# Kernel optimization log

Hardware: AMD Instinct MI355X
Metric: run time of the kernel (lower is better)

Reference implementation:

```python
import jax, jax.numpy as jnp
import numpy as np

TAU = 2.0          # LIF membrane time constant (spikingjelly default)
V_TH = 1.0         # v_threshold
V_RESET = 0.0      # hard reset value
ATAN_ALPHA = 2.0   # surrogate.ATan default alpha
EPS = 1e-12        # F.normalize eps

@jax.custom_vjp
def spike_fn(x):
    # Heaviside forward, ATan surrogate backward
    return (x >= 0).astype(x.dtype)

def _spike_fwd(x):
    return spike_fn(x), x

def _spike_bwd(x, g):
    sg = (ATAN_ALPHA / 2.0) / (1.0 + (jnp.pi / 2.0 * ATAN_ALPHA * x) ** 2)
    return (g * sg,)

spike_fn.defvjp(_spike_fwd, _spike_bwd)

def setup_inputs() -> dict:
    key = jax.random.key(0)
    k1, k2 = jax.random.split(key)
    T, B, F, H = 32, 512, 2048, 2048
    x_seq = jax.random.normal(k1, (T, B, F), dtype=jnp.float32)
    lim = float(np.sqrt(6.0 / (F + H)))  # xavier_uniform
    W = jax.random.uniform(k2, (H, F), dtype=jnp.float32, minval=-lim, maxval=lim)
    b = jnp.zeros((H,), dtype=jnp.float32)
    return {"x_seq": x_seq, "W": W, "b": b}

def reference(x_seq, W, b):
    # Linear: [T,B,F] @ [F,H] -> [T,B,H]
    cur = jnp.einsum('tbf,hf->tbh', x_seq, W) + b
    # F.normalize(dim=-1): L2 normalize the injected current per neuron vector
    norm = jnp.maximum(jnp.sqrt(jnp.sum(cur * cur, axis=-1, keepdims=True)), EPS)
    cur = cur / norm

    def step(v, c):
        # LIF charge: v <- v + (x - (v - v_reset)) / tau
        v = v + (c - (v - V_RESET)) / TAU
        s = spike_fn(v - V_TH)
        sd = jax.lax.stop_gradient(s)  # detach_reset=True
        v = v * (1.0 - sd) + V_RESET * sd  # hard reset
        return v, s

    v0 = jnp.zeros(cur.shape[1:], dtype=cur.dtype)  # [B,H]
    _, spk_seq = jax.lax.scan(step, v0, cur)  # spk_seq: [T,B,H]
    count = spk_seq.sum(axis=0)  # [B,H]
    return spk_seq, count
```

## Files before the change

kernel.cpp:

```cpp
#include <hip/hip_runtime.h>
#include <hip/hip_bf16.h>

#define T_SZ 32
#define B_SZ 512
#define F_SZ 2048
#define H_SZ 2048
#define M_SZ (T_SZ * B_SZ)

#define BM 256
#define BN 256
#define BK 128
#define NT (F_SZ / BK)
#define BUF_BYTES  65536
#define HALF_BYTES 16384

typedef int   i32x8  __attribute__((ext_vector_type(8)));
typedef float f32x16 __attribute__((ext_vector_type(16)));

__device__ __forceinline__ void gload_lds16(const void* g, void* l) {
    __builtin_amdgcn_global_load_lds(
        (const __attribute__((address_space(1))) unsigned int*)g,
        (__attribute__((address_space(3))) unsigned int*)l,
        16, 0, 0);
}

__device__ __forceinline__ float bf16_bits_to_f32(unsigned short u) {
    return __uint_as_float(((unsigned)u) << 16);
}

__device__ __forceinline__ void sbar() {
    __builtin_amdgcn_sched_barrier(0);
    __builtin_amdgcn_s_barrier();
    __builtin_amdgcn_sched_barrier(0);
}

__device__ __forceinline__ void stage_half_tile(unsigned char* lds,
                                                const unsigned char* gpanel,
                                                int kbyte, int tid) {
    #pragma unroll
    for (int j = 0; j < 2; ++j) {
        int c   = j * 512 + tid;
        int row = c >> 3;
        int u   = (c & 7) ^ (row & 7);
        gload_lds16(gpanel + (size_t)row * F_SZ + kbyte + u * 16, (void*)(lds + c * 16));
    }
}

__global__ __launch_bounds__(256) void cvt_fp8_kernel(const float* __restrict__ in,
                                                      unsigned int* __restrict__ out,
                                                      float scale, int n8) {
    int i = blockIdx.x * 256 + threadIdx.x;
    if (i >= n8) return;
    float4 v0 = ((const float4*)in)[2 * i];
    float4 v1 = ((const float4*)in)[2 * i + 1];
    int w0 = __builtin_amdgcn_cvt_pk_fp8_f32(v0.x * scale, v0.y * scale, 0, false);
    w0     = __builtin_amdgcn_cvt_pk_fp8_f32(v0.z * scale, v0.w * scale, w0, true);
    int w1 = __builtin_amdgcn_cvt_pk_fp8_f32(v1.x * scale, v1.y * scale, 0, false);
    w1     = __builtin_amdgcn_cvt_pk_fp8_f32(v1.z * scale, v1.w * scale, w1, true);
    ((uint2*)out)[i] = make_uint2((unsigned)w0, (unsigned)w1);
}

__global__ __launch_bounds__(256) void init_ss_kernel(float4* __restrict__ ss4) {
    ss4[blockIdx.x * 256 + threadIdx.x] = make_float4(0.f, 0.f, 0.f, 0.f);
}

__global__ __launch_bounds__(512, 2) void gemm_fp8_kernel(const unsigned char* __restrict__ A,
                                                          const unsigned char* __restrict__ Bt,
                                                          const float* __restrict__ bias,
                                                          __hip_bfloat16* __restrict__ C,
                                                          float* __restrict__ ss)
{
    __shared__ __align__(16) unsigned char smem[2 * BUF_BYTES];

    const int tid  = threadIdx.x;
    const int lane = tid & 63;
    const int wave = tid >> 6;
    const int wm   = wave >> 2;
    const int wn   = wave & 3;
    const int l31  = lane & 31;
    const int kh   = lane >> 5;

    const int flat = blockIdx.y * 8 + blockIdx.x;
    const int swz  = (flat & 7) * 64 + (flat >> 3);
    const int n0   = (swz & 7) * BN;
    const int m0   = (swz >> 3) * BM;

    f32x16 acc[4][2] = {};

    stage_half_tile(smem + 32768,              Bt + (size_t)(n0      ) * F_SZ, 0, tid);
    stage_half_tile(smem + 32768 + HALF_BYTES, Bt + (size_t)(n0 + 128) * F_SZ, 0, tid);
    stage_half_tile(smem,                      A  + (size_t)(m0      ) * F_SZ, 0, tid);
    stage_half_tile(smem + HALF_BYTES,         A  + (size_t)(m0 + 128) * F_SZ, 0, tid);
    stage_half_tile(smem + BUF_BYTES + 32768,              Bt + (size_t)(n0      ) * F_SZ, BK, tid);
    stage_half_tile(smem + BUF_BYTES + 32768 + HALF_BYTES, Bt + (size_t)(n0 + 128) * F_SZ, BK, tid);
    asm volatile("s_waitcnt vmcnt(4)" ::: "memory");
    sbar();

    #pragma unroll 1
    for (int kt = 0; kt < NT; ++kt) {
        const int cur = kt & 1;
        const int nxt = cur ^ 1;
        unsigned char* const As = smem + cur * BUF_BYTES;
        unsigned char* const Bs = As + 32768;

        auto read_af = [&](i32x8* dst, int mi) {
            const int ra = wm * 128 + mi * 32 + l31;
            #pragma unroll
            for (int s = 0; s < 2; ++s) {
                const int ua = s * 4 + kh * 2;
                ((int4*)&dst[s])[0] = *(const int4*)(As + ra * BK + (((ua + 0) ^ (ra & 7)) * 16));
                ((int4*)&dst[s])[1] = *(const int4*)(As + ra * BK + (((ua + 1) ^ (ra & 7)) * 16));
            }
        };

        i32x8 bq[2][2];
        #pragma unroll
        for (int ni = 0; ni < 2; ++ni) {
            const int rb = wn * 64 + ni * 32 + l31;
            #pragma unroll
            for (int s = 0; s < 2; ++s) {
                const int ua = s * 4 + kh * 2;
                ((int4*)&bq[ni][s])[0] = *(const int4*)(Bs + rb * BK + (((ua + 0) ^ (rb & 7)) * 16));
                ((int4*)&bq[ni][s])[1] = *(const int4*)(Bs + rb * BK + (((ua + 1) ^ (rb & 7)) * 16));
            }
        }
        i32x8 af[2][2];
        read_af(af[0], 0);

        #pragma unroll
        for (int mi = 0; mi < 4; ++mi) {
            if (mi < 3) read_af(af[(mi + 1) & 1], mi + 1);

            if (mi == 0 && kt < NT - 1)
                stage_half_tile(smem + nxt * BUF_BYTES,              A  + (size_t)(m0      ) * F_SZ, (kt + 1) * BK, tid);
            if (mi == 1 && kt < NT - 1)
                stage_half_tile(smem + nxt * BUF_BYTES + HALF_BYTES, A  + (size_t)(m0 + 128) * F_SZ, (kt + 1) * BK, tid);
            if (mi == 2 && kt < NT - 2)
                stage_half_tile(smem + cur * BUF_BYTES + 32768,              Bt + (size_t)(n0      ) * F_SZ, (kt + 2) * BK, tid);
            if (mi == 3 && kt < NT - 2)
                stage_half_tile(smem + cur * BUF_BYTES + 32768 + HALF_BYTES, Bt + (size_t)(n0 + 128) * F_SZ, (kt + 2) * BK, tid);

            __builtin_amdgcn_sched_barrier(0);
            __builtin_amdgcn_s_setprio(1);
            #pragma unroll
            for (int ni = 0; ni < 2; ++ni)
                #pragma unroll
                for (int s = 0; s < 2; ++s)
                    acc[mi][ni] = __builtin_amdgcn_mfma_scale_f32_32x32x64_f8f6f4(
                        af[mi & 1][s], bq[ni][s], acc[mi][ni],
                        0 , 0 ,
                        0, 0x7f7f7f7f,
                        0, 0x7f7f7f7f);
            __builtin_amdgcn_s_setprio(0);
            if (mi < 3) sbar();
        }

        if (kt <= NT - 3)      { asm volatile("s_waitcnt vmcnt(4)" ::: "memory"); }
        else if (kt == NT - 2) { asm volatile("s_waitcnt vmcnt(0)" ::: "memory"); }
        sbar();
    }

    float bv[2];
    #pragma unroll
    for (int ni = 0; ni < 2; ++ni) bv[ni] = bias[n0 + wn * 64 + ni * 32 + l31];
    #pragma unroll
    for (int mi = 0; mi < 4; ++mi) {
        const int gmb = m0 + wm * 128 + mi * 32 + 4 * kh;
        #pragma unroll
        for (int r = 0; r < 16; ++r) {
            const int grow = gmb + (r & 3) + 8 * (r >> 2);
            float p = 0.f;
            #pragma unroll
            for (int ni = 0; ni < 2; ++ni) {
                const int gn = n0 + wn * 64 + ni * 32 + l31;
                const float val = acc[mi][ni][r] * (1.0f / 256.0f) + bv[ni];
                C[(size_t)grow * H_SZ + gn] = __float2bfloat16(val);
                p += val * val;
            }
            p += __shfl_xor(p, 1, 64);
            p += __shfl_xor(p, 2, 64);
            p += __shfl_xor(p, 4, 64);
            p += __shfl_xor(p, 8, 64);
            p += __shfl_xor(p, 16, 64);
            if (l31 == 0) atomicAdd(ss + grow, p);
        }
    }
}

__global__ __launch_bounds__(256) void lif_scan_kernel(const __hip_bfloat16* __restrict__ cur,
                                                       const float* __restrict__ ss,
                                                       float* __restrict__ spk,
                                                       float* __restrict__ cnt)
{
    __shared__ float s_inv[T_SZ];
    const int gid = blockIdx.x * 256 + threadIdx.x;
    const int b   = gid >> 9;
    const int h0  = (gid & 511) * 4;

    if (threadIdx.x < T_SZ)
        s_inv[threadIdx.x] = 1.0f / fmaxf(sqrtf(ss[threadIdx.x * B_SZ + b]), 1e-12f);
    __syncthreads();

    const size_t stride = (size_t)B_SZ * H_SZ;
    const size_t base   = (size_t)b * H_SZ + h0;
    const __hip_bfloat16* p = cur + base;

    ushort4 pk[3];
    pk[0] = *(const ushort4*)(p);
    pk[1] = *(const ushort4*)(p + stride);
    pk[2] = *(const ushort4*)(p + 2 * stride);

    float v[4]  = {0, 0, 0, 0};
    float cn[4] = {0, 0, 0, 0};
    #pragma unroll
    for (int t = 0; t < T_SZ; ++t) {
        const ushort4 k = pk[t % 3];
        if (t + 3 < T_SZ) pk[t % 3] = *(const ushort4*)(p + (size_t)(t + 3) * stride);
        const float inv = s_inv[t];
        float so[4];
        {
            float c;
            c = bf16_bits_to_f32(k.x) * inv; v[0] += (c - v[0]) * 0.5f;
            c = bf16_bits_to_f32(k.y) * inv; v[1] += (c - v[1]) * 0.5f;
            c = bf16_bits_to_f32(k.z) * inv; v[2] += (c - v[2]) * 0.5f;
            c = bf16_bits_to_f32(k.w) * inv; v[3] += (c - v[3]) * 0.5f;
        }
        #pragma unroll
        for (int j = 0; j < 4; ++j) {
            float s = (v[j] >= 1.0f) ? 1.0f : 0.0f;
            so[j] = s;
            cn[j] += s;
            v[j] = (s != 0.f) ? 0.f : v[j];
        }
        *(float4*)(spk + base + (size_t)t * stride) = make_float4(so[0], so[1], so[2], so[3]);
    }
    *(float4*)(cnt + base) = make_float4(cn[0], cn[1], cn[2], cn[3]);
}

extern "C" void kernel_launch(void* const* d_in, const int* in_sizes, int n_in,
                              void* d_out, int out_size, void* d_ws, size_t ws_size,
                              hipStream_t stream) {
    const float* x    = (const float*)d_in[0];
    const float* W    = (const float*)d_in[1];
    const float* bias = (const float*)d_in[2];

    float* spk = (float*)d_out;
    float* cnt = spk + (size_t)T_SZ * B_SZ * H_SZ;

    char* ws = (char*)d_ws;
    unsigned char* x8    = (unsigned char*)ws;
    unsigned char* W8    = x8 + (size_t)M_SZ * F_SZ;
    __hip_bfloat16* curb = (__hip_bfloat16*)(W8 + (size_t)H_SZ * F_SZ);
    float* ss            = (float*)((char*)curb + (size_t)M_SZ * H_SZ * 2);

    init_ss_kernel<<<M_SZ / 1024, 256, 0, stream>>>((float4*)ss);
    cvt_fp8_kernel<<<(M_SZ * F_SZ / 8) / 256, 256, 0, stream>>>(x, (unsigned int*)x8, 1.0f,   M_SZ * F_SZ / 8);
    cvt_fp8_kernel<<<(H_SZ * F_SZ / 8) / 256, 256, 0, stream>>>(W, (unsigned int*)W8, 256.0f, H_SZ * F_SZ / 8);
    gemm_fp8_kernel<<<dim3(H_SZ / BN, M_SZ / BM), 512, 0, stream>>>(x8, W8, bias, curb, ss);
    lif_scan_kernel<<<(B_SZ * H_SZ / 4) / 256, 256, 0, stream>>>(curb, ss, spk, cnt);
}
```

Baseline: 372.2 us.

## Shrink FP8 GEMM tile to 256x128x64 with 4 waves and precomputed LDS offsets

Rebuilds the FP8 GEMM mainloop around a smaller 256x128 output tile with BK=64, 256 threads (4 waves, 2x2), and a 4-way XOR swizzle instead of 8-way. Staging and LDS read offsets are computed once before the loop. The per-K schedule is split into two MFMA halves, with the next A tile and the B tile two steps ahead issued between them. The smaller block and LDS footprint aim for more resident blocks and finer-grained latency hiding, at the cost of less operand reuse per block, twice as many K iterations and barriers, and more global traffic for A.

```diff
diff --git a/kernel.cpp b/kernel.cpp
--- a/kernel.cpp
+++ b/kernel.cpp
@@ -8,11 +8,12 @@
 #define M_SZ (T_SZ * B_SZ)
 
 #define BM 256
-#define BN 256
-#define BK 128
+#define BN 128
+#define BK 64
 #define NT (F_SZ / BK)
-#define BUF_BYTES  65536
-#define HALF_BYTES 16384
+#define ABYTES (BM * BK)
+#define BBYTES (BN * BK)
+#define TILE_BYTES (ABYTES + BBYTES)
 
 typedef int   i32x8  __attribute__((ext_vector_type(8)));
 typedef float f32x16 __attribute__((ext_vector_type(16)));
@@ -34,17 +35,8 @@
     __builtin_amdgcn_sched_barrier(0);
 }
 
-__device__ __forceinline__ void stage_half_tile(unsigned char* lds,
-                                                const unsigned char* gpanel,
-                                                int kbyte, int tid) {
-    #pragma unroll
-    for (int j = 0; j < 2; ++j) {
-        int c   = j * 512 + tid;
-        int row = c >> 3;
-        int u   = (c & 7) ^ (row & 7);
-        gload_lds16(gpanel + (size_t)row * F_SZ + kbyte + u * 16, (void*)(lds + c * 16));
-    }
-}
+#define MFMA_FP8(a, b, c) __builtin_amdgcn_mfma_scale_f32_32x32x64_f8f6f4( \
+        (a), (b), (c), 0 , 0 , 0, 0x7f7f7f7f, 0, 0x7f7f7f7f)
 
 __global__ __launch_bounds__(256) void cvt_fp8_kernel(const float* __restrict__ in,
                                                       unsigned int* __restrict__ out,
@@ -64,100 +56,128 @@
     ss4[blockIdx.x * 256 + threadIdx.x] = make_float4(0.f, 0.f, 0.f, 0.f);
 }
 
-__global__ __launch_bounds__(512, 2) void gemm_fp8_kernel(const unsigned char* __restrict__ A,
+__global__ __launch_bounds__(256, 2) void gemm_fp8_kernel(const unsigned char* __restrict__ A,
                                                           const unsigned char* __restrict__ Bt,
                                                           const float* __restrict__ bias,
                                                           __hip_bfloat16* __restrict__ C,
                                                           float* __restrict__ ss)
 {
-    __shared__ __align__(16) unsigned char smem[2 * BUF_BYTES];
+    __shared__ __align__(16) unsigned char smem[2 * TILE_BYTES];
 
     const int tid  = threadIdx.x;
     const int lane = tid & 63;
     const int wave = tid >> 6;
-    const int wm   = wave >> 2;
-    const int wn   = wave & 3;
+    const int wm   = wave >> 1;
+    const int wn   = wave & 1;
     const int l31  = lane & 31;
     const int kh   = lane >> 5;
 
-    const int flat = blockIdx.y * 8 + blockIdx.x;
-    const int swz  = (flat & 7) * 64 + (flat >> 3);
-    const int n0   = (swz & 7) * BN;
-    const int m0   = (swz >> 3) * BM;
+    const int flat = blockIdx.y * 16 + blockIdx.x;
+    const int swz  = (flat & 7) * 128 + (flat >> 3);
+    const int n0   = (swz & 15) * BN;
+    const int m0   = (swz >> 4) * BM;
+
+    const unsigned char* const Ap = A  + (size_t)m0 * F_SZ;
+    const unsigned char* const Bp = Bt + (size_t)n0 * F_SZ;
+
+    int sAg[4], sAl[4];
+    #pragma unroll
+    for (int j = 0; j < 4; ++j) {
+        const int c = j * 256 + tid;
+        const int row = c >> 2;
+        const int u = (c & 3) ^ (row & 3);
+        sAg[j] = row * F_SZ + u * 16;
+        sAl[j] = c * 16;
+    }
+    int sBg[2], sBl[2];
+    #pragma unroll
+    for (int j = 0; j < 2; ++j) {
+        const int c = j * 256 + tid;
+        const int row = c >> 2;
+        const int u = (c & 3) ^ (row & 3);
+        sBg[j] = row * F_SZ + u * 16;
+        sBl[j] = c * 16;
+    }
+
+    int aoff[4][2], boff[2][2];
+    #pragma unroll
+    for (int mi = 0; mi < 4; ++mi) {
+        const int ra = wm * 128 + mi * 32 + l31;
+        #pragma unroll
+        for (int j = 0; j < 2; ++j)
+            aoff[mi][j] = ra * BK + (((kh * 2 + j) ^ (ra & 3)) * 16);
+    }
+    #pragma unroll
+    for (int ni = 0; ni < 2; ++ni) {
+        const int rb = wn * 64 + ni * 32 + l31;
+        #pragma unroll
+        for (int j = 0; j < 2; ++j)
+            boff[ni][j] = rb * BK + (((kh * 2 + j) ^ (rb & 3)) * 16);
+    }
+
+    auto stageA = [&](int p, int kt) {
+        unsigned char* const d = smem + p * TILE_BYTES;
+        #pragma unroll
+        for (int j = 0; j < 4; ++j) gload_lds16(Ap + kt * BK + sAg[j], d + sAl[j]);
+    };
+    auto stageB = [&](int p, int kt) {
+        unsigned char* const d = smem + p * TILE_BYTES + ABYTES;
+        #pragma unroll
+        for (int j = 0; j < 2; ++j) gload_lds16(Bp + kt * BK + sBg[j], d + sBl[j]);
+    };
 
     f32x16 acc[4][2] = {};
 
-    stage_half_tile(smem + 32768,              Bt + (size_t)(n0      ) * F_SZ, 0, tid);
-    stage_half_tile(smem + 32768 + HALF_BYTES, Bt + (size_t)(n0 + 128) * F_SZ, 0, tid);
-    stage_half_tile(smem,                      A  + (size_t)(m0      ) * F_SZ, 0, tid);
-    stage_half_tile(smem + HALF_BYTES,         A  + (size_t)(m0 + 128) * F_SZ, 0, tid);
-    stage_half_tile(smem + BUF_BYTES + 32768,              Bt + (size_t)(n0      ) * F_SZ, BK, tid);
-    stage_half_tile(smem + BUF_BYTES + 32768 + HALF_BYTES, Bt + (size_t)(n0 + 128) * F_SZ, BK, tid);
-    asm volatile("s_waitcnt vmcnt(4)" ::: "memory");
+    stageB(0, 0);
+    stageA(0, 0);
+    stageB(1, 1);
+    asm volatile("s_waitcnt vmcnt(2)" ::: "memory");
     sbar();
 
     #pragma unroll 1
     for (int kt = 0; kt < NT; ++kt) {
-        const int cur = kt & 1;
-        const int nxt = cur ^ 1;
-        unsigned char* const As = smem + cur * BUF_BYTES;
-        unsigned char* const Bs = As + 32768;
-
-        auto read_af = [&](i32x8* dst, int mi) {
-            const int ra = wm * 128 + mi * 32 + l31;
-            #pragma unroll
-            for (int s = 0; s < 2; ++s) {
-                const int ua = s * 4 + kh * 2;
-                ((int4*)&dst[s])[0] = *(const int4*)(As + ra * BK + (((ua + 0) ^ (ra & 7)) * 16));
-                ((int4*)&dst[s])[1] = *(const int4*)(As + ra * BK + (((ua + 1) ^ (ra & 7)) * 16));
-            }
-        };
-
-        i32x8 bq[2][2];
+        unsigned char* const buf = smem + (kt & 1) * TILE_BYTES;
+        unsigned char* const Bs  = buf + ABYTES;
+
+        i32x8 a01[2], a23[2], bq[2];
+
         #pragma unroll
         for (int ni = 0; ni < 2; ++ni) {
-            const int rb = wn * 64 + ni * 32 + l31;
-            #pragma unroll
-            for (int s = 0; s < 2; ++s) {
-                const int ua = s * 4 + kh * 2;
-                ((int4*)&bq[ni][s])[0] = *(const int4*)(Bs + rb * BK + (((ua + 0) ^ (rb & 7)) * 16));
-                ((int4*)&bq[ni][s])[1] = *(const int4*)(Bs + rb * BK + (((ua + 1) ^ (rb & 7)) * 16));
-            }
-        }
-        i32x8 af[2][2];
-        read_af(af[0], 0);
-
-        #pragma unroll
-        for (int mi = 0; mi < 4; ++mi) {
-            if (mi < 3) read_af(af[(mi + 1) & 1], mi + 1);
-
-            if (mi == 0 && kt < NT - 1)
-                stage_half_tile(smem + nxt * BUF_BYTES,              A  + (size_t)(m0      ) * F_SZ, (kt + 1) * BK, tid);
-            if (mi == 1 && kt < NT - 1)
-                stage_half_tile(smem + nxt * BUF_BYTES + HALF_BYTES, A  + (size_t)(m0 + 128) * F_SZ, (kt + 1) * BK, tid);
-            if (mi == 2 && kt < NT - 2)
-                stage_half_tile(smem + cur * BUF_BYTES + 32768,              Bt + (size_t)(n0      ) * F_SZ, (kt + 2) * BK, tid);
-            if (mi == 3 && kt < NT - 2)
-                stage_half_tile(smem + cur * BUF_BYTES + 32768 + HALF_BYTES, Bt + (size_t)(n0 + 128) * F_SZ, (kt + 2) * BK, tid);
-
-            __builtin_amdgcn_sched_barrier(0);
-            __builtin_amdgcn_s_setprio(1);
-            #pragma unroll
-            for (int ni = 0; ni < 2; ++ni)
-                #pragma unroll
-                for (int s = 0; s < 2; ++s)
-                    acc[mi][ni] = __builtin_amdgcn_mfma_scale_f32_32x32x64_f8f6f4(
-                        af[mi & 1][s], bq[ni][s], acc[mi][ni],
-                        0 , 0 ,
-                        0, 0x7f7f7f7f,
-                        0, 0x7f7f7f7f);
-            __builtin_amdgcn_s_setprio(0);
-            if (mi < 3) sbar();
-        }
-
-        if (kt <= NT - 3)      { asm volatile("s_waitcnt vmcnt(4)" ::: "memory"); }
+            ((int4*)&bq[ni])[0] = *(const int4*)(Bs + boff[ni][0]);
+            ((int4*)&bq[ni])[1] = *(const int4*)(Bs + boff[ni][1]);
+        }
+        #pragma unroll
+        for (int mi = 0; mi < 2; ++mi) {
+            ((int4*)&a01[mi])[0] = *(const int4*)(buf + aoff[mi][0]);
+            ((int4*)&a01[mi])[1] = *(const int4*)(buf + aoff[mi][1]);
+        }
+        if (kt + 1 < NT) stageA((kt + 1) & 1, kt + 1);
+
+        __builtin_amdgcn_s_setprio(1);
+        acc[0][0] = MFMA_FP8(a01[0], bq[0], acc[0][0]);
+        acc[0][1] = MFMA_FP8(a01[0], bq[1], acc[0][1]);
+        acc[1][0] = MFMA_FP8(a01[1], bq[0], acc[1][0]);
+        acc[1][1] = MFMA_FP8(a01[1], bq[1], acc[1][1]);
+        __builtin_amdgcn_s_setprio(0);
+        sbar();
+
+        #pragma unroll
+        for (int mi = 0; mi < 2; ++mi) {
+            ((int4*)&a23[mi])[0] = *(const int4*)(buf + aoff[2 + mi][0]);
+            ((int4*)&a23[mi])[1] = *(const int4*)(buf + aoff[2 + mi][1]);
+        }
+        if (kt + 2 < NT) stageB(kt & 1, kt + 2);
+
+        __builtin_amdgcn_s_setprio(1);
+        acc[2][0] = MFMA_FP8(a23[0], bq[0], acc[2][0]);
+        acc[2][1] = MFMA_FP8(a23[0], bq[1], acc[2][1]);
+        acc[3][0] = MFMA_FP8(a23[1], bq[0], acc[3][0]);
+        acc[3][1] = MFMA_FP8(a23[1], bq[1], acc[3][1]);
+        __builtin_amdgcn_s_setprio(0);
+
+        if (kt < NT - 2)       { asm volatile("s_waitcnt vmcnt(2)" ::: "memory"); }
         else if (kt == NT - 2) { asm volatile("s_waitcnt vmcnt(0)" ::: "memory"); }
-        sbar();
+        if (kt < NT - 1) sbar();
     }
 
     float bv[2];
@@ -256,6 +276,6 @@
     init_ss_kernel<<<M_SZ / 1024, 256, 0, stream>>>((float4*)ss);
     cvt_fp8_kernel<<<(M_SZ * F_SZ / 8) / 256, 256, 0, stream>>>(x, (unsigned int*)x8, 1.0f,   M_SZ * F_SZ / 8);
     cvt_fp8_kernel<<<(H_SZ * F_SZ / 8) / 256, 256, 0, stream>>>(W, (unsigned int*)W8, 256.0f, H_SZ * F_SZ / 8);
-    gemm_fp8_kernel<<<dim3(H_SZ / BN, M_SZ / BM), 512, 0, stream>>>(x8, W8, bias, curb, ss);
+    gemm_fp8_kernel<<<dim3(H_SZ / BN, M_SZ / BM), 256, 0, stream>>>(x8, W8, bias, curb, ss);
     lif_scan_kernel<<<(B_SZ * H_SZ / 4) / 256, 256, 0, stream>>>(curb, ss, spk, cnt);
 }
```

Result: no change. 373.3 us (+0.3%).

## Restructure FP8 GEMM main loop into eight k-split phases with per-phase staging

Applied to the files above, without the earlier changes.

Splits each 128-wide K tile into two 64-byte subtiles stored in separate LDS regions with a new 4-chunk XOR swizzle. The inner loop becomes eight phases, each loading one A fragment (and B fragments on the first phase of a subtile), issuing one global-to-LDS copy, and running two MFMAs between barriers. The old scheme that prefetched B two tiles ahead is replaced by a simple double buffer one tile ahead. Offsets are precomputed outside the loop to cut address arithmetic. In exchange there are twice as many barriers per tile plus a full lgkmcnt wait before each MFMA pair, which may serialise LDS reads with compute.

```diff
diff --git a/kernel.cpp b/kernel.cpp
--- a/kernel.cpp
+++ b/kernel.cpp
@@ -11,8 +11,8 @@
 #define BN 256
 #define BK 128
 #define NT (F_SZ / BK)
-#define BUF_BYTES  65536
-#define HALF_BYTES 16384
+#define SUB_BYTES 16384
+#define BUF_BYTES 65536
 
 typedef int   i32x8  __attribute__((ext_vector_type(8)));
 typedef float f32x16 __attribute__((ext_vector_type(16)));
@@ -34,17 +34,12 @@
     __builtin_amdgcn_sched_barrier(0);
 }
 
-__device__ __forceinline__ void stage_half_tile(unsigned char* lds,
-                                                const unsigned char* gpanel,
-                                                int kbyte, int tid) {
-    #pragma unroll
-    for (int j = 0; j < 2; ++j) {
-        int c   = j * 512 + tid;
-        int row = c >> 3;
-        int u   = (c & 7) ^ (row & 7);
-        gload_lds16(gpanel + (size_t)row * F_SZ + kbyte + u * 16, (void*)(lds + c * 16));
-    }
-}
+#define LGKM0 do { asm volatile("s_waitcnt lgkmcnt(0)" ::: "memory"); \
+                   __builtin_amdgcn_sched_barrier(0); } while (0)
+#define VMW(n) asm volatile("s_waitcnt vmcnt(" #n ")" ::: "memory")
+
+#define MFMA_FP8(a, b, c) __builtin_amdgcn_mfma_scale_f32_32x32x64_f8f6f4( \
+        (a), (b), (c), 0 , 0 , 0, 0x7f7f7f7f, 0, 0x7f7f7f7f)
 
 __global__ __launch_bounds__(256) void cvt_fp8_kernel(const float* __restrict__ in,
                                                       unsigned int* __restrict__ out,
@@ -85,79 +80,100 @@
     const int n0   = (swz & 7) * BN;
     const int m0   = (swz >> 3) * BM;
 
+    const unsigned char* const Ap = A  + (size_t)m0 * F_SZ;
+    const unsigned char* const Bp = Bt + (size_t)n0 * F_SZ;
+
+    int gOff[2], lOff[2];
+    #pragma unroll
+    for (int pr = 0; pr < 2; ++pr) {
+        const int idx = pr * 512 + tid;
+        const int row = idx >> 2;
+        const int u   = (idx & 3) ^ ((row >> 1) & 3);
+        gOff[pr] = row * F_SZ + u * 16;
+        lOff[pr] = idx * 16;
+    }
+
+    int aoffb[4][2], boffb[2][2];
+    #pragma unroll
+    for (int mi = 0; mi < 4; ++mi) {
+        const int ra = wm * 128 + mi * 32 + l31;
+        #pragma unroll
+        for (int j = 0; j < 2; ++j)
+            aoffb[mi][j] = ra * 64 + (((kh * 2 + j) ^ ((ra >> 1) & 3)) * 16);
+    }
+    #pragma unroll
+    for (int ni = 0; ni < 2; ++ni) {
+        const int rb = wn * 64 + ni * 32 + l31;
+        #pragma unroll
+        for (int j = 0; j < 2; ++j)
+            boffb[ni][j] = rb * 64 + (((kh * 2 + j) ^ ((rb >> 1) & 3)) * 16);
+    }
+
     f32x16 acc[4][2] = {};
-
-    stage_half_tile(smem + 32768,              Bt + (size_t)(n0      ) * F_SZ, 0, tid);
-    stage_half_tile(smem + 32768 + HALF_BYTES, Bt + (size_t)(n0 + 128) * F_SZ, 0, tid);
-    stage_half_tile(smem,                      A  + (size_t)(m0      ) * F_SZ, 0, tid);
-    stage_half_tile(smem + HALF_BYTES,         A  + (size_t)(m0 + 128) * F_SZ, 0, tid);
-    stage_half_tile(smem + BUF_BYTES + 32768,              Bt + (size_t)(n0      ) * F_SZ, BK, tid);
-    stage_half_tile(smem + BUF_BYTES + 32768 + HALF_BYTES, Bt + (size_t)(n0 + 128) * F_SZ, BK, tid);
-    asm volatile("s_waitcnt vmcnt(4)" ::: "memory");
-    sbar();
+    i32x8 bq[2];
+
+    {
+        unsigned char* const d = smem;
+        #pragma unroll
+        for (int ks = 0; ks < 2; ++ks)
+            #pragma unroll
+            for (int pr = 0; pr < 2; ++pr) {
+                gload_lds16(Ap + ks * 64 + gOff[pr], d + ks * SUB_BYTES + lOff[pr]);
+                gload_lds16(Bp + ks * 64 + gOff[pr], d + 2 * SUB_BYTES + ks * SUB_BYTES + lOff[pr]);
+            }
+        VMW(0);
+        sbar();
+    }
 
     #pragma unroll 1
     for (int kt = 0; kt < NT; ++kt) {
-        const int cur = kt & 1;
-        const int nxt = cur ^ 1;
-        unsigned char* const As = smem + cur * BUF_BYTES;
-        unsigned char* const Bs = As + 32768;
-
-        auto read_af = [&](i32x8* dst, int mi) {
-            const int ra = wm * 128 + mi * 32 + l31;
-            #pragma unroll
-            for (int s = 0; s < 2; ++s) {
-                const int ua = s * 4 + kh * 2;
-                ((int4*)&dst[s])[0] = *(const int4*)(As + ra * BK + (((ua + 0) ^ (ra & 7)) * 16));
-                ((int4*)&dst[s])[1] = *(const int4*)(As + ra * BK + (((ua + 1) ^ (ra & 7)) * 16));
-            }
-        };
-
-        i32x8 bq[2][2];
-        #pragma unroll
-        for (int ni = 0; ni < 2; ++ni) {
-            const int rb = wn * 64 + ni * 32 + l31;
-            #pragma unroll
-            for (int s = 0; s < 2; ++s) {
-                const int ua = s * 4 + kh * 2;
-                ((int4*)&bq[ni][s])[0] = *(const int4*)(Bs + rb * BK + (((ua + 0) ^ (rb & 7)) * 16));
-                ((int4*)&bq[ni][s])[1] = *(const int4*)(Bs + rb * BK + (((ua + 1) ^ (rb & 7)) * 16));
-            }
-        }
-        i32x8 af[2][2];
-        read_af(af[0], 0);
-
-        #pragma unroll
-        for (int mi = 0; mi < 4; ++mi) {
-            if (mi < 3) read_af(af[(mi + 1) & 1], mi + 1);
-
-            if (mi == 0 && kt < NT - 1)
-                stage_half_tile(smem + nxt * BUF_BYTES,              A  + (size_t)(m0      ) * F_SZ, (kt + 1) * BK, tid);
-            if (mi == 1 && kt < NT - 1)
-                stage_half_tile(smem + nxt * BUF_BYTES + HALF_BYTES, A  + (size_t)(m0 + 128) * F_SZ, (kt + 1) * BK, tid);
-            if (mi == 2 && kt < NT - 2)
-                stage_half_tile(smem + cur * BUF_BYTES + 32768,              Bt + (size_t)(n0      ) * F_SZ, (kt + 2) * BK, tid);
-            if (mi == 3 && kt < NT - 2)
-                stage_half_tile(smem + cur * BUF_BYTES + 32768 + HALF_BYTES, Bt + (size_t)(n0 + 128) * F_SZ, (kt + 2) * BK, tid);
-
-            __builtin_amdgcn_sched_barrier(0);
-            __builtin_amdgcn_s_setprio(1);
-            #pragma unroll
-            for (int ni = 0; ni < 2; ++ni)
-                #pragma unroll
-                for (int s = 0; s < 2; ++s)
-                    acc[mi][ni] = __builtin_amdgcn_mfma_scale_f32_32x32x64_f8f6f4(
-                        af[mi & 1][s], bq[ni][s], acc[mi][ni],
-                        0 , 0 ,
-                        0, 0x7f7f7f7f,
-                        0, 0x7f7f7f7f);
-            __builtin_amdgcn_s_setprio(0);
-            if (mi < 3) sbar();
-        }
-
-        if (kt <= NT - 3)      { asm volatile("s_waitcnt vmcnt(4)" ::: "memory"); }
-        else if (kt == NT - 2) { asm volatile("s_waitcnt vmcnt(0)" ::: "memory"); }
-        sbar();
+        const unsigned char* const buf = smem + (kt & 1) * BUF_BYTES;
+        unsigned char* const nb        = smem + ((kt + 1) & 1) * BUF_BYTES;
+        const bool stg = (kt + 1 < NT);
+        const int  kb  = (kt + 1) * BK;
+
+#define STG_A(ks, pr) do { if (stg) gload_lds16(Ap + kb + (ks) * 64 + gOff[pr], \
+                                                nb + (ks) * SUB_BYTES + lOff[pr]); } while (0)
+#define STG_B(ks, pr) do { if (stg) gload_lds16(Bp + kb + (ks) * 64 + gOff[pr], \
+                                                nb + 2 * SUB_BYTES + (ks) * SUB_BYTES + lOff[pr]); } while (0)
+
+#define PHASE(ks, mi, STAGE_STMT, PRE_TRAIL) do {                              \
+        i32x8 aw;                                                              \
+        if ((mi) == 0) {                                                       \
+            const unsigned char* Bb = buf + 2 * SUB_BYTES + (ks) * SUB_BYTES;  \
+            ((int4*)&bq[0])[0] = *(const int4*)(Bb + boffb[0][0]);             \
+            ((int4*)&bq[0])[1] = *(const int4*)(Bb + boffb[0][1]);             \
+            ((int4*)&bq[1])[0] = *(const int4*)(Bb + boffb[1][0]);             \
+            ((int4*)&bq[1])[1] = *(const int4*)(Bb + boffb[1][1]);             \
+        }                                                                      \
+        {                                                                      \
+            const unsigned char* Ab = buf + (ks) * SUB_BYTES;                  \
+            ((int4*)&aw)[0] = *(const int4*)(Ab + aoffb[mi][0]);               \
+            ((int4*)&aw)[1] = *(const int4*)(Ab + aoffb[mi][1]);               \
+        }                                                                      \
+        STAGE_STMT;                                                            \
+        sbar();                        \
+        LGKM0;                                                                 \
+        __builtin_amdgcn_s_setprio(1);                                         \
+        acc[mi][0] = MFMA_FP8(aw, bq[0], acc[mi][0]);                          \
+        acc[mi][1] = MFMA_FP8(aw, bq[1], acc[mi][1]);                          \
+        __builtin_amdgcn_s_setprio(0);                                         \
+        PRE_TRAIL;                                                             \
+        sbar();                                          \
+    } while (0)
+
+        PHASE(0, 0, STG_A(0, 0), );
+        PHASE(0, 1, STG_B(0, 0), );
+        PHASE(0, 2, STG_A(0, 1), );
+        PHASE(0, 3, STG_B(0, 1), { if (kt != NT - 1) { VMW(4); } else { VMW(0); } });
+        PHASE(1, 0, STG_A(1, 0), );
+        PHASE(1, 1, STG_B(1, 0), );
+        PHASE(1, 2, STG_A(1, 1), );
+        PHASE(1, 3, STG_B(1, 1), { if (kt < NT - 1) { VMW(4); } });
+
+#undef PHASE
+#undef STG_A
+#undef STG_B
     }
 
     float bv[2];
```

New measurement: 393.1 us. +5.6%, slower.
